# Optimization experiments

Measured on AMD Instinct MI355X. Metric: run time of the kernel, lower is better.

Reference implementation:

```python
import jax, jax.numpy as jnp
import numpy as np

N, C, W_DIM, H_DIM = 2, 256, 64, 64
HEADS = 4
DH = C // HEADS  # per-head dim for Q,K,V projections
EPS = 1e-5


def _layernorm(x, w, b):
    mu = jnp.mean(x, axis=-1, keepdims=True)
    var = jnp.var(x, axis=-1, keepdims=True)
    return (x - mu) * jax.lax.rsqrt(var + EPS) * w + b


def setup_inputs() -> dict:
    key = jax.random.key(0)
    ks = jax.random.split(key, 12)
    s = 1.0 / np.sqrt(C)
    return {
        "x": jax.random.normal(ks[0], (N, C, W_DIM, H_DIM), dtype=jnp.float32),
        "ln1_w": jnp.ones((C,), jnp.float32),
        "ln1_b": jnp.zeros((C,), jnp.float32),
        # per-head projection weights, laid out for x @ W: [heads, C, DH]
        "WQ": jax.random.normal(ks[1], (HEADS, C, DH), jnp.float32) * s,
        "WK": jax.random.normal(ks[2], (HEADS, C, DH), jnp.float32) * s,
        "WV": jax.random.normal(ks[3], (HEADS, C, DH), jnp.float32) * s,
        "ln2_w": jnp.ones((C,), jnp.float32),
        "ln2_b": jnp.zeros((C,), jnp.float32),
        "W1": jax.random.normal(ks[4], (C, C), jnp.float32) * s,
        "b1": jnp.zeros((C,), jnp.float32),
        "W2": jax.random.normal(ks[5], (C, C), jnp.float32) * s,
        "b2": jnp.zeros((C,), jnp.float32),
    }


def reference(x, ln1_w, ln1_b, WQ, WK, WV, ln2_w, ln2_b, W1, b1, W2, b2):
    n, c, w, h = x.shape
    s = w * h
    # 'n c w h -> n (w h) c'
    r = x.reshape(n, c, s).transpose(0, 2, 1)          # [n, s, c]
    norm = _layernorm(r, ln1_w, ln1_b)
    # all heads at once (original loops over heads)
    Q = jnp.einsum('nsc,hcd->nhsd', norm, WQ)
    K = jnp.einsum('nsc,hcd->nhsd', norm, WK)
    V = jnp.einsum('nsc,hcd->nhsd', norm, WV)
    # scale is 1/sqrt(seq_len) per original (keys.shape[1])
    y = jnp.einsum('nhqd,nhkd->nhqk', Q, K) / jnp.sqrt(jnp.float32(s))
    # QUIRK: softmax over dim=1 of [n, q, k] => the QUERY axis (axis=2 here)
    z = jax.nn.softmax(y, axis=2)
    attn = jnp.einsum('nhqk,nhkd->nhqd', z, V)         # [n, h, s, dh]
    attn_cat = attn.transpose(0, 2, 1, 3).reshape(n, s, c)
    out = attn_cat + r
    out = _layernorm(out, ln2_w, ln2_b)
    out = jax.nn.gelu(out @ W1 + b1, approximate=False) @ W2 + b2
    out = out + attn_cat
    # 'n (w h) c -> n c w h'
    return out.transpose(0, 2, 1).reshape(n, c, w, h)
```

## Files before the change

kernel.cpp:

```cpp
#include <hip/hip_runtime.h>
#include <math.h>

#define SEQ 4096
#define CH  256
#define NHT 8
#define DHD 64

#define QSCALE 0.0225421092f

using bf16x8 = __attribute__((ext_vector_type(8))) short;
using f32x4  = __attribute__((ext_vector_type(4))) float;
typedef unsigned short u16;
typedef unsigned int   u32;

__device__ __forceinline__ u16 f2bf(float f) {
    u32 u = __float_as_uint(f);
    u = (u + 0x7fffu + ((u >> 16) & 1u)) >> 16;
    return (u16)u;
}
__device__ __forceinline__ float bf2f(u16 h) {
    return __uint_as_float(((u32)h) << 16);
}
__device__ __forceinline__ float fexp2(float x) {
    return __builtin_amdgcn_exp2f(x);
}

__global__ __launch_bounds__(256) void k_prep(const float* __restrict__ x,
                                              const float* __restrict__ ln1w,
                                              const float* __restrict__ ln1b,
                                              const float* __restrict__ WQ,
                                              const float* __restrict__ WK,
                                              const float* __restrict__ WV,
                                              const float* __restrict__ W1,
                                              const float* __restrict__ W2,
                                              u16* __restrict__ norm,
                                              u16* __restrict__ BtQKV,
                                              u16* __restrict__ W1t,
                                              u16* __restrict__ W2t)
{
    __shared__ float tile[32][257];
    __shared__ float mu[32], rs[32];
    int bid = blockIdx.x;
    int t = threadIdx.x;
    if (bid < 1280) {
        int id = bid * 256 + t;
        if (id < 768 * 256) {
            int j = id >> 8, c = id & 255;
            int which = j >> 8, h = (j >> 6) & 3, d = j & 63;
            const float* W = (which == 0) ? WQ : (which == 1) ? WK : WV;
            BtQKV[id] = f2bf(W[(h * 256 + c) * 64 + d]);
        } else if (id < 768 * 256 + 65536) {
            int jj = id - 768 * 256;
            int j = jj >> 8, c = jj & 255;
            W1t[jj] = f2bf(W1[c * 256 + j]);
        } else if (id < 768 * 256 + 2 * 65536) {
            int jj = id - 768 * 256 - 65536;
            int j = jj >> 8, c = jj & 255;
            W2t[jj] = f2bf(W2[c * 256 + j]);
        }
        return;
    }
    int b2i = bid - 1280;
    int n = b2i >> 7, s0 = (b2i & 127) * 32;
    int sl = t & 31, cg = t >> 5;
    for (int cc = 0; cc < 256; cc += 8) {
        int c = cc + cg;
        tile[sl][c] = x[(n * 256 + c) * SEQ + s0 + sl];
    }
    __syncthreads();
    int wv = t >> 6, l = t & 63;
    for (int rr = 0; rr < 8; rr++) {
        int s = wv * 8 + rr;
        float a0 = tile[s][l], a1 = tile[s][l + 64], a2 = tile[s][l + 128], a3 = tile[s][l + 192];
        float sm = a0 + a1 + a2 + a3;
        float sq = a0 * a0 + a1 * a1 + a2 * a2 + a3 * a3;
        for (int off = 32; off; off >>= 1) { sm += __shfl_xor(sm, off); sq += __shfl_xor(sq, off); }
        if (l == 0) {
            float m = sm * (1.f / 256.f);
            mu[s] = m;
            rs[s] = rsqrtf(sq * (1.f / 256.f) - m * m + 1e-5f);
        }
    }
    __syncthreads();
    float ww = ln1w[t], bb = ln1b[t];
    for (int s = 0; s < 32; s++) {
        float v = (tile[s][t] - mu[s]) * rs[s] * ww + bb;
        norm[(n * SEQ + s0 + s) * 256 + t] = f2bf(v);
    }
}

__global__ __launch_bounds__(256) void k_qkv(const u16* __restrict__ norm,
                                             const u16* __restrict__ Bt,
                                             u16* __restrict__ Qo,
                                             u16* __restrict__ Ko,
                                             float* __restrict__ Vfo)
{
    int m0 = blockIdx.x * 64, j0 = blockIdx.y * 128;
    int t = threadIdx.x, w = t >> 6, lane = t & 63, quad = lane >> 4, l16 = lane & 15;
    const u16* Ap = norm + (long)(m0 + w * 16 + l16) * 256;
    const u16* Bp = Bt + (long)j0 * 256;
    f32x4 z = {0.f, 0.f, 0.f, 0.f};
    f32x4 acc[8];
    #pragma unroll
    for (int j = 0; j < 8; j++) acc[j] = z;
    #pragma unroll
    for (int kc = 0; kc < 8; kc++) {
        bf16x8 a = *(const bf16x8*)&Ap[kc * 32 + quad * 8];
        #pragma unroll
        for (int j = 0; j < 8; j++) {
            bf16x8 b = *(const bf16x8*)&Bp[(long)(j * 16 + l16) * 256 + kc * 32 + quad * 8];
            acc[j] = __builtin_amdgcn_mfma_f32_16x16x32_bf16(a, b, acc[j], 0, 0, 0);
        }
    }
    #pragma unroll
    for (int j = 0; j < 8; j++) {
        int col = j0 + j * 16 + l16;
        int which = col >> 8, h = (col >> 6) & 3, d = col & 63;
        int m = m0 + w * 16 + quad * 4;
        int n = m >> 12, s = m & 4095;
        if (which == 2) {
            float4 o = make_float4(acc[j][0], acc[j][1], acc[j][2], acc[j][3]);
            *(float4*)&Vfo[((long)(n * 4 + h) * 64 + d) * SEQ + s] = o;
        } else {
            u16* dst = (which == 0) ? Qo : Ko;
            float sc = (which == 0) ? QSCALE : 1.0f;
            #pragma unroll
            for (int r = 0; r < 4; r++)
                dst[((n * 4 + h) * SEQ + s + r) * 64 + d] = f2bf(acc[j][r] * sc);
        }
    }
}

__device__ __forceinline__ void xcd_decode(int s, int& g, int& sub) {
    int xcd = s & 7, m = s >> 3;
    g = xcd * 2 + (m >> 5);
    sub = m & 31;
}

__global__ __launch_bounds__(256) void k_pass1(const u16* __restrict__ Q,
                                               const u16* __restrict__ Km,
                                               float* __restrict__ D2)
{
    __shared__ float Dred[128];
    int g, sub;
    xcd_decode(blockIdx.x, g, sub);
    int nh = g & 7, qc = g >> 3, k0 = sub * 128;
    const u16* Qh = Q + (long)nh * SEQ * 64;
    const u16* Kh = Km + (long)nh * SEQ * 64;
    int t = threadIdx.x, w = t >> 6, lane = t & 63, quad = lane >> 4, l16 = lane & 15;
    bf16x8 Kf[8][2];
    #pragma unroll
    for (int i = 0; i < 8; i++) {
        Kf[i][0] = *(const bf16x8*)&Kh[(k0 + i * 16 + l16) * 64 + quad * 8];
        Kf[i][1] = *(const bf16x8*)&Kh[(k0 + i * 16 + l16) * 64 + 32 + quad * 8];
    }
    if (t < 128) Dred[t] = 0.f;
    f32x4 z = {0.f, 0.f, 0.f, 0.f};
    float Dacc[8][4] = {};
    const int qw0 = qc * 2048 + w * 512;

#define P1_LOADQ(B0, B1, ST)                                                  \
    {                                                                         \
        int _q = qw0 + (ST) * 16 + l16;                                       \
        B0 = *(const bf16x8*)&Qh[_q * 64 + quad * 8];                         \
        B1 = *(const bf16x8*)&Qh[_q * 64 + 32 + quad * 8];                    \
    }
#define P1_STEP(B0, B1)                                                       \
    {                                                                         \
        _Pragma("unroll")                                                     \
        for (int i = 0; i < 8; i++) {                                         \
            f32x4 acc = z;                                                    \
            acc = __builtin_amdgcn_mfma_f32_16x16x32_bf16(Kf[i][0], B0, acc, 0, 0, 0); \
            acc = __builtin_amdgcn_mfma_f32_16x16x32_bf16(Kf[i][1], B1, acc, 0, 0, 0); \
            _Pragma("unroll")                                                 \
            for (int r = 0; r < 4; r++) Dacc[i][r] += fexp2(acc[r]);          \
        }                                                                     \
    }

    bf16x8 qa0, qa1, qb0, qb1;
    P1_LOADQ(qa0, qa1, 0)
    P1_LOADQ(qb0, qb1, 1)
    for (int st = 0; st < 32; st += 2) {
        P1_STEP(qa0, qa1)
        if (st + 2 < 32) { P1_LOADQ(qa0, qa1, st + 2) }
        P1_STEP(qb0, qb1)
        if (st + 3 < 32) { P1_LOADQ(qb0, qb1, st + 3) }
    }
#undef P1_LOADQ
#undef P1_STEP

    #pragma unroll
    for (int i = 0; i < 8; i++)
        #pragma unroll
        for (int r = 0; r < 4; r++) {
            float v = Dacc[i][r];
            v += __shfl_xor(v, 1); v += __shfl_xor(v, 2);
            v += __shfl_xor(v, 4); v += __shfl_xor(v, 8);
            Dacc[i][r] = v;
        }
    __syncthreads();
    if (l16 == 0) {
        #pragma unroll
        for (int i = 0; i < 8; i++)
            #pragma unroll
            for (int r = 0; r < 4; r++)
                atomicAdd(&Dred[i * 16 + quad * 4 + r], Dacc[i][r]);
    }
    __syncthreads();
    if (t < 128) D2[((long)(qc * NHT + nh)) * SEQ + k0 + t] = Dred[t];
}

__global__ __launch_bounds__(256) void k_vdiv(const float* __restrict__ Vf,
                                              const float* __restrict__ D2,
                                              u16* __restrict__ Vto)
{
    int b = blockIdx.x;
    int nh = b >> 6, d = b & 63;
    const float* Da = D2 + (long)nh * SEQ;
    const float* Db = Da + (long)NHT * SEQ;
    const float* src = Vf + ((long)nh * 64 + d) * SEQ;
    u16* dst = Vto + ((long)nh * 64 + d) * SEQ;
    int t = threadIdx.x;
    #pragma unroll
    for (int half = 0; half < 2; half++) {
        int k = half * 2048 + t * 8;
        float4 va = *(const float4*)&src[k];
        float4 vb = *(const float4*)&src[k + 4];
        float4 a0 = *(const float4*)&Da[k], a1 = *(const float4*)&Da[k + 4];
        float4 b0 = *(const float4*)&Db[k], b1 = *(const float4*)&Db[k + 4];
        float o[8];
        o[0] = va.x / (a0.x + b0.x); o[1] = va.y / (a0.y + b0.y);
        o[2] = va.z / (a0.z + b0.z); o[3] = va.w / (a0.w + b0.w);
        o[4] = vb.x / (a1.x + b1.x); o[5] = vb.y / (a1.y + b1.y);
        o[6] = vb.z / (a1.z + b1.z); o[7] = vb.w / (a1.w + b1.w);
        uint4 pk;
        pk.x = (u32)f2bf(o[0]) | ((u32)f2bf(o[1]) << 16);
        pk.y = (u32)f2bf(o[2]) | ((u32)f2bf(o[3]) << 16);
        pk.z = (u32)f2bf(o[4]) | ((u32)f2bf(o[5]) << 16);
        pk.w = (u32)f2bf(o[6]) | ((u32)f2bf(o[7]) << 16);
        *(uint4*)&dst[k] = pk;
    }
}

__global__ __launch_bounds__(256, 1) void k_pass2(const u16* __restrict__ Q,
                                                  const u16* __restrict__ Km,
                                                  const u16* __restrict__ Vt,
                                                  float* __restrict__ acat2)
{
    __shared__ __align__(16) u16 lP[4][128][36];
    float (*red)[68] = (float(*)[68])lP;

    int g, sub;
    xcd_decode(blockIdx.x, g, sub);
    int nh = g & 7, kcid = g >> 3, q0 = sub * 128;
    int n = nh >> 2, h = nh & 3;
    const u16* Qh = Q + (long)nh * SEQ * 64;
    const u16* Kh = Km + (long)nh * SEQ * 64;
    const u16* Vh = Vt + (long)nh * 64 * SEQ;
    int t = threadIdx.x, w = t >> 6, lane = t & 63, quad = lane >> 4, l16 = lane & 15;
    const int kw0 = kcid * 2048 + w * 512;

    bf16x8 Qf[8][2];
    #pragma unroll
    for (int jq = 0; jq < 8; jq++)
        #pragma unroll
        for (int ch = 0; ch < 2; ch++)
            Qf[jq][ch] = *(const bf16x8*)&Qh[(q0 + jq * 16 + l16) * 64 + ch * 32 + quad * 8];

    f32x4 z = {0.f, 0.f, 0.f, 0.f};
    f32x4 accO[8][4];
    #pragma unroll
    for (int jq = 0; jq < 8; jq++)
        #pragma unroll
        for (int jd = 0; jd < 4; jd++) accO[jq][jd] = z;

#define LOAD_K(KA, KPOS)                                                      \
    {                                                                         \
        _Pragma("unroll")                                                     \
        for (int ksub = 0; ksub < 2; ksub++) {                                \
            KA[ksub][0] = *(const bf16x8*)&Kh[((KPOS) + ksub * 16 + l16) * 64 + quad * 8];      \
            KA[ksub][1] = *(const bf16x8*)&Kh[((KPOS) + ksub * 16 + l16) * 64 + 32 + quad * 8]; \
        }                                                                     \
    }
#define LOAD_V(VB, KPOS)                                                      \
    {                                                                         \
        _Pragma("unroll")                                                     \
        for (int jd = 0; jd < 4; jd++)                                        \
            VB[jd] = *(const bf16x8*)&Vh[(jd * 16 + l16) * SEQ + (KPOS) + quad * 8]; \
    }
#define QK_SLAB(KA)                                                           \
    {                                                                         \
        _Pragma("unroll")                                                     \
        for (int ksub = 0; ksub < 2; ksub++) {                                \
            _Pragma("unroll")                                                 \
            for (int jq = 0; jq < 8; jq++) {                                  \
                f32x4 acc = z;                                                \
                acc = __builtin_amdgcn_mfma_f32_16x16x32_bf16(KA[ksub][0], Qf[jq][0], acc, 0, 0, 0); \
                acc = __builtin_amdgcn_mfma_f32_16x16x32_bf16(KA[ksub][1], Qf[jq][1], acc, 0, 0, 0); \
                u32 e0 = __float_as_uint(fexp2(acc[0]));                      \
                u32 e1 = __float_as_uint(fexp2(acc[1]));                      \
                u32 e2 = __float_as_uint(fexp2(acc[2]));                      \
                u32 e3 = __float_as_uint(fexp2(acc[3]));                      \
                uint2 pk;                                                     \
                pk.x = __builtin_amdgcn_perm(e1, e0, 0x07060302u);            \
                pk.y = __builtin_amdgcn_perm(e3, e2, 0x07060302u);            \
                *(uint2*)&lP[w][jq * 16 + l16][ksub * 16 + quad * 4] = pk;    \
            }                                                                 \
        }                                                                     \
    }
#define PV_SLAB(VB)                                                           \
    {                                                                         \
        _Pragma("unroll")                                                     \
        for (int jq = 0; jq < 8; jq++) {                                      \
            bf16x8 pa = *(const bf16x8*)&lP[w][jq * 16 + l16][quad * 8];      \
            _Pragma("unroll")                                                 \
            for (int jd = 0; jd < 4; jd++)                                    \
                accO[jq][jd] = __builtin_amdgcn_mfma_f32_16x16x32_bf16(pa, VB[jd], accO[jq][jd], 0, 0, 0); \
        }                                                                     \
    }

    bf16x8 kA0[2][2], kA1[2][2], vb0[4], vb1[4];
    LOAD_K(kA0, kw0)
    LOAD_V(vb0, kw0)
    LOAD_K(kA1, kw0 + 32)
    LOAD_V(vb1, kw0 + 32)

    for (int tt = 0; tt < 8; tt++) {
        int kf = kw0 + tt * 64;
        QK_SLAB(kA0)
        if (tt < 7) { LOAD_K(kA0, kf + 64) }
        PV_SLAB(vb0)
        if (tt < 7) { LOAD_V(vb0, kf + 64) }
        QK_SLAB(kA1)
        if (tt < 7) { LOAD_K(kA1, kf + 96) }
        PV_SLAB(vb1)
        if (tt < 7) { LOAD_V(vb1, kf + 96) }
    }
#undef LOAD_K
#undef LOAD_V
#undef QK_SLAB
#undef PV_SLAB

    __syncthreads();
    for (int src = 0; src < 4; src++) {
        if (w == src) {
            #pragma unroll
            for (int jq = 0; jq < 8; jq++)
                #pragma unroll
                for (int jd = 0; jd < 4; jd++)
                    #pragma unroll
                    for (int r = 0; r < 4; r++) {
                        float* cell = &red[jq * 16 + quad * 4 + r][jd * 16 + l16];
                        if (src == 0) *cell = accO[jq][jd][r];
                        else          *cell += accO[jq][jd][r];
                    }
        }
        __syncthreads();
    }
    float* dst = acat2 + (long)kcid * 8192 * 256;
    #pragma unroll
    for (int p = 0; p < 8; p++) {
        int row = p * 16 + (t >> 4);
        int ch = (t & 15) * 4;
        float4 o = *(float4*)&red[row][ch];
        *(float4*)&dst[((long)n * SEQ + q0 + row) * 256 + h * 64 + ch] = o;
    }
}

__global__ __launch_bounds__(256) void k_tail(const float* __restrict__ x,
                                              const float* __restrict__ acat2,
                                              const float* __restrict__ lnw,
                                              const float* __restrict__ lnb,
                                              const u16* __restrict__ W1t,
                                              const float* __restrict__ b1v,
                                              const u16* __restrict__ W2t,
                                              const float* __restrict__ b2v,
                                              float* __restrict__ out)
{
    __shared__ __align__(16) unsigned char smem[16448];
    float (*tile)[257] = (float(*)[257])smem;
    u16 (*lT)[264] = (u16(*)[264])smem;
    __shared__ float aF[16][257];
    __shared__ float mu[16], rs[16];
    __shared__ __align__(16) u16 lH[16][264];

    const long STRIDE = (long)8192 * 256;
    int m0 = blockIdx.x * 16;
    int n = m0 >> 12, s0 = m0 & 4095;
    int t = threadIdx.x, w = t >> 6, lane = t & 63, quad = lane >> 4, l16 = lane & 15;

    {
        int sl = t & 15, cg = t >> 4;
        for (int cc = 0; cc < 256; cc += 16) {
            int c = cc + cg;
            tile[sl][c] = x[(n * 256 + c) * SEQ + s0 + sl];
        }
    }
    __syncthreads();
    for (int s = 0; s < 16; s++) {
        long idx = (long)(m0 + s) * 256 + t;
        float a = acat2[idx] + acat2[idx + STRIDE];
        aF[s][t] = a;
        tile[s][t] += a;
    }
    __syncthreads();
    {
        int l = t & 63;
        for (int rr = 0; rr < 4; rr++) {
            int s = w * 4 + rr;
            float a0 = tile[s][l], a1 = tile[s][l + 64], a2 = tile[s][l + 128], a3 = tile[s][l + 192];
            float sm = a0 + a1 + a2 + a3;
            float sq = a0 * a0 + a1 * a1 + a2 * a2 + a3 * a3;
            for (int off = 32; off; off >>= 1) { sm += __shfl_xor(sm, off); sq += __shfl_xor(sq, off); }
            if (l == 0) {
                float m = sm * (1.f / 256.f);
                mu[s] = m;
                rs[s] = rsqrtf(sq * (1.f / 256.f) - m * m + 1e-5f);
            }
        }
    }
    __syncthreads();
    {
        float ww = lnw[t], bb = lnb[t];
        for (int s = 0; s < 16; s++)
            lH[s][t] = f2bf((tile[s][t] - mu[s]) * rs[s] * ww + bb);
    }
    __syncthreads();

    f32x4 z = {0.f, 0.f, 0.f, 0.f};
    f32x4 acc1[4];
    #pragma unroll
    for (int js = 0; js < 4; js++) acc1[js] = z;
    #pragma unroll
    for (int kc = 0; kc < 8; kc++) {
        bf16x8 b = *(const bf16x8*)&lH[l16][kc * 32 + quad * 8];
        #pragma unroll
        for (int js = 0; js < 4; js++) {
            bf16x8 a = *(const bf16x8*)&W1t[(long)(w * 64 + js * 16 + l16) * 256 + kc * 32 + quad * 8];
            acc1[js] = __builtin_amdgcn_mfma_f32_16x16x32_bf16(a, b, acc1[js], 0, 0, 0);
        }
    }
    #pragma unroll
    for (int js = 0; js < 4; js++) {
        u32 e[4];
        #pragma unroll
        for (int r = 0; r < 4; r++) {
            int j = w * 64 + js * 16 + quad * 4 + r;
            float v = acc1[js][r] + b1v[j];
            float g = 0.5f * v * (1.f + erff(v * 0.70710678118f));
            u32 u = __float_as_uint(g);
            e[r] = u + 0x7fffu + ((u >> 16) & 1u);
        }
        uint2 pk;
        pk.x = __builtin_amdgcn_perm(e[1], e[0], 0x07060302u);
        pk.y = __builtin_amdgcn_perm(e[3], e[2], 0x07060302u);
        *(uint2*)&lT[l16][w * 64 + js * 16 + quad * 4] = pk;
    }
    __syncthreads();
    f32x4 acc2[4];
    #pragma unroll
    for (int cs = 0; cs < 4; cs++) acc2[cs] = z;
    #pragma unroll
    for (int kc = 0; kc < 8; kc++) {
        bf16x8 pa = *(const bf16x8*)&lT[l16][kc * 32 + quad * 8];
        #pragma unroll
        for (int cs = 0; cs < 4; cs++) {
            bf16x8 wb = *(const bf16x8*)&W2t[(long)(w * 64 + cs * 16 + l16) * 256 + kc * 32 + quad * 8];
            acc2[cs] = __builtin_amdgcn_mfma_f32_16x16x32_bf16(pa, wb, acc2[cs], 0, 0, 0);
        }
    }
    #pragma unroll
    for (int cs = 0; cs < 4; cs++) {
        int c = w * 64 + cs * 16 + l16;
        float bj = b2v[c];
        float vv[4];
        #pragma unroll
        for (int r = 0; r < 4; r++)
            vv[r] = acc2[cs][r] + bj + aF[quad * 4 + r][c];
        float4 o = make_float4(vv[0], vv[1], vv[2], vv[3]);
        *(float4*)&out[((long)n * 256 + c) * SEQ + s0 + quad * 4] = o;
    }
}

extern "C" void kernel_launch(void* const* d_in, const int* in_sizes, int n_in,
                              void* d_out, int out_size, void* d_ws, size_t ws_size,
                              hipStream_t stream) {
    const float* x    = (const float*)d_in[0];
    const float* ln1w = (const float*)d_in[1];
    const float* ln1b = (const float*)d_in[2];
    const float* WQ   = (const float*)d_in[3];
    const float* WK   = (const float*)d_in[4];
    const float* WV   = (const float*)d_in[5];
    const float* ln2w = (const float*)d_in[6];
    const float* ln2b = (const float*)d_in[7];
    const float* W1   = (const float*)d_in[8];
    const float* b1   = (const float*)d_in[9];
    const float* W2   = (const float*)d_in[10];
    const float* b2   = (const float*)d_in[11];
    float* out = (float*)d_out;

    char* p = (char*)d_ws;
    u16* norm   = (u16*)p;   p += (size_t)8192 * 256 * 2;
    u16* BtQKV  = (u16*)p;   p += (size_t)768 * 256 * 2;
    u16* W1t    = (u16*)p;   p += (size_t)256 * 256 * 2;
    u16* W2t    = (u16*)p;   p += (size_t)256 * 256 * 2;
    u16* Qb     = (u16*)p;   p += (size_t)NHT * SEQ * 64 * 2;
    u16* Kb     = (u16*)p;   p += (size_t)NHT * SEQ * 64 * 2;
    u16* VtT    = (u16*)p;   p += (size_t)NHT * SEQ * 64 * 2;
    float* D2   = (float*)p; p += (size_t)2 * NHT * SEQ * 4;
    float* acat2= (float*)p; p += (size_t)2 * 8192 * 256 * 4;
    float* Vf   = acat2;

    k_prep<<<1536, 256, 0, stream>>>(x, ln1w, ln1b, WQ, WK, WV, W1, W2,
                                     norm, BtQKV, W1t, W2t);
    k_qkv<<<dim3(128, 6), 256, 0, stream>>>(norm, BtQKV, Qb, Kb, Vf);
    k_pass1<<<512, 256, 0, stream>>>(Qb, Kb, D2);
    k_vdiv<<<512, 256, 0, stream>>>(Vf, D2, VtT);
    k_pass2<<<512, 256, 0, stream>>>(Qb, Kb, VtT, acat2);
    k_tail<<<512, 256, 0, stream>>>(x, acat2, ln2w, ln2b, W1t, b1, W2t, b2, out);
}
```

Baseline: 236.8 us.

## Split attention work by query rows per wave instead of key chunks

Each wave in k_pass2 now owns 32 of the block's 128 query rows and walks all 2048 keys of its key chunk, where before every wave covered all 128 queries over a quarter of the keys. This removes the serialized cross-wave LDS reduction and its barriers, and shrinks the accumulator and Q-fragment register footprint so launch bounds can allow two blocks per CU. The cost is that each wave loads K and V for four times as many keys, with less reuse of each K/V fragment per MFMA, which raises global/L2 traffic.

```diff
diff --git a/kernel.cpp b/kernel.cpp
--- a/kernel.cpp
+++ b/kernel.cpp
@@ -242,13 +242,12 @@
     }
 }
 
-__global__ __launch_bounds__(256, 1) void k_pass2(const u16* __restrict__ Q,
+__global__ __launch_bounds__(256, 2) void k_pass2(const u16* __restrict__ Q,
                                                   const u16* __restrict__ Km,
                                                   const u16* __restrict__ Vt,
                                                   float* __restrict__ acat2)
 {
-    __shared__ __align__(16) u16 lP[4][128][36];
-    float (*red)[68] = (float(*)[68])lP;
+    __shared__ __align__(16) unsigned char smem[34816];
 
     int g, sub;
     xcd_decode(blockIdx.x, g, sub);
@@ -258,19 +257,22 @@
     const u16* Kh = Km + (long)nh * SEQ * 64;
     const u16* Vh = Vt + (long)nh * 64 * SEQ;
     int t = threadIdx.x, w = t >> 6, lane = t & 63, quad = lane >> 4, l16 = lane & 15;
-    const int kw0 = kcid * 2048 + w * 512;
-
-    bf16x8 Qf[8][2];
-    #pragma unroll
-    for (int jq = 0; jq < 8; jq++)
+    u16 (*lP)[36]  = (u16(*)[36])(smem + w * 8704);
+    float (*red)[68] = (float(*)[68])(smem + w * 8704);
+    const int kw0 = kcid * 2048;
+    const int qofs = w * 32;
+
+    bf16x8 Qf[2][2];
+    #pragma unroll
+    for (int jq = 0; jq < 2; jq++)
         #pragma unroll
         for (int ch = 0; ch < 2; ch++)
-            Qf[jq][ch] = *(const bf16x8*)&Qh[(q0 + jq * 16 + l16) * 64 + ch * 32 + quad * 8];
+            Qf[jq][ch] = *(const bf16x8*)&Qh[(q0 + qofs + jq * 16 + l16) * 64 + ch * 32 + quad * 8];
 
     f32x4 z = {0.f, 0.f, 0.f, 0.f};
-    f32x4 accO[8][4];
-    #pragma unroll
-    for (int jq = 0; jq < 8; jq++)
+    f32x4 accO[2][4];
+    #pragma unroll
+    for (int jq = 0; jq < 2; jq++)
         #pragma unroll
         for (int jd = 0; jd < 4; jd++) accO[jq][jd] = z;
 
@@ -293,7 +295,7 @@
         _Pragma("unroll")                                                     \
         for (int ksub = 0; ksub < 2; ksub++) {                                \
             _Pragma("unroll")                                                 \
-            for (int jq = 0; jq < 8; jq++) {                                  \
+            for (int jq = 0; jq < 2; jq++) {                                  \
                 f32x4 acc = z;                                                \
                 acc = __builtin_amdgcn_mfma_f32_16x16x32_bf16(KA[ksub][0], Qf[jq][0], acc, 0, 0, 0); \
                 acc = __builtin_amdgcn_mfma_f32_16x16x32_bf16(KA[ksub][1], Qf[jq][1], acc, 0, 0, 0); \
@@ -304,15 +306,15 @@
                 uint2 pk;                                                     \
                 pk.x = __builtin_amdgcn_perm(e1, e0, 0x07060302u);            \
                 pk.y = __builtin_amdgcn_perm(e3, e2, 0x07060302u);            \
-                *(uint2*)&lP[w][jq * 16 + l16][ksub * 16 + quad * 4] = pk;    \
+                *(uint2*)&lP[jq * 16 + l16][ksub * 16 + quad * 4] = pk;       \
             }                                                                 \
         }                                                                     \
     }
 #define PV_SLAB(VB)                                                           \
     {                                                                         \
         _Pragma("unroll")                                                     \
-        for (int jq = 0; jq < 8; jq++) {                                      \
-            bf16x8 pa = *(const bf16x8*)&lP[w][jq * 16 + l16][quad * 8];      \
+        for (int jq = 0; jq < 2; jq++) {                                      \
+            bf16x8 pa = *(const bf16x8*)&lP[jq * 16 + l16][quad * 8];         \
             _Pragma("unroll")                                                 \
             for (int jd = 0; jd < 4; jd++)                                    \
                 accO[jq][jd] = __builtin_amdgcn_mfma_f32_16x16x32_bf16(pa, VB[jd], accO[jq][jd], 0, 0, 0); \
@@ -325,45 +327,36 @@
     LOAD_K(kA1, kw0 + 32)
     LOAD_V(vb1, kw0 + 32)
 
-    for (int tt = 0; tt < 8; tt++) {
+    for (int tt = 0; tt < 32; tt++) {
         int kf = kw0 + tt * 64;
         QK_SLAB(kA0)
-        if (tt < 7) { LOAD_K(kA0, kf + 64) }
+        if (tt < 31) { LOAD_K(kA0, kf + 64) }
         PV_SLAB(vb0)
-        if (tt < 7) { LOAD_V(vb0, kf + 64) }
+        if (tt < 31) { LOAD_V(vb0, kf + 64) }
         QK_SLAB(kA1)
-        if (tt < 7) { LOAD_K(kA1, kf + 96) }
+        if (tt < 31) { LOAD_K(kA1, kf + 96) }
         PV_SLAB(vb1)
-        if (tt < 7) { LOAD_V(vb1, kf + 96) }
+        if (tt < 31) { LOAD_V(vb1, kf + 96) }
     }
 #undef LOAD_K
 #undef LOAD_V
 #undef QK_SLAB
 #undef PV_SLAB
 
-    __syncthreads();
-    for (int src = 0; src < 4; src++) {
-        if (w == src) {
+    #pragma unroll
+    for (int jq = 0; jq < 2; jq++)
+        #pragma unroll
+        for (int jd = 0; jd < 4; jd++)
             #pragma unroll
-            for (int jq = 0; jq < 8; jq++)
-                #pragma unroll
-                for (int jd = 0; jd < 4; jd++)
-                    #pragma unroll
-                    for (int r = 0; r < 4; r++) {
-                        float* cell = &red[jq * 16 + quad * 4 + r][jd * 16 + l16];
-                        if (src == 0) *cell = accO[jq][jd][r];
-                        else          *cell += accO[jq][jd][r];
-                    }
-        }
-        __syncthreads();
-    }
+            for (int r = 0; r < 4; r++)
+                red[jq * 16 + quad * 4 + r][jd * 16 + l16] = accO[jq][jd][r];
     float* dst = acat2 + (long)kcid * 8192 * 256;
     #pragma unroll
     for (int p = 0; p < 8; p++) {
-        int row = p * 16 + (t >> 4);
-        int ch = (t & 15) * 4;
+        int row = p * 4 + quad;
+        int ch = l16 * 4;
         float4 o = *(float4*)&red[row][ch];
-        *(float4*)&dst[((long)n * SEQ + q0 + row) * 256 + h * 64 + ch] = o;
+        *(float4*)&dst[((long)n * SEQ + q0 + qofs + row) * 256 + h * 64 + ch] = o;
     }
 }
 
```

Result: slower. 293.3 us (+23.9%).
